# Kernel tuning notes

Measured on AMD Instinct MI355X. Metric: run time of the kernel, lower is better.

Reference implementation:

```python
import jax, jax.numpy as jnp
import numpy as np

N_NODES = 50000
N_EDGES = 800000
N_GRAPHS = 64
HEADS = 4
IN_CH, HID_CH, OUT_CH = 128, 64, 32


def setup_inputs() -> dict:
    key = jax.random.key(0)
    ks = jax.random.split(key, 13)
    x = jax.random.normal(ks[0], (N_NODES, IN_CH), dtype=jnp.float32)
    edge_index = jax.random.randint(ks[1], (2, N_EDGES), 0, N_NODES, dtype=jnp.int64)
    tensor_batch = jnp.sort(jax.random.randint(ks[2], (N_NODES,), 0, N_GRAPHS, dtype=jnp.int64))
    s = 0.1
    return {
        "x": x,
        "edge_index": edge_index,
        "tensor_batch": tensor_batch,
        "W1": jax.random.normal(ks[3], (IN_CH, HEADS * HID_CH), dtype=jnp.float32) * s,
        "a_src1": jax.random.normal(ks[4], (HEADS, HID_CH), dtype=jnp.float32) * s,
        "a_dst1": jax.random.normal(ks[5], (HEADS, HID_CH), dtype=jnp.float32) * s,
        "b1": jnp.zeros((HEADS * HID_CH,), dtype=jnp.float32),
        "W2": jax.random.normal(ks[6], (HEADS * HID_CH, HEADS * OUT_CH), dtype=jnp.float32) * s,
        "a_src2": jax.random.normal(ks[7], (HEADS, OUT_CH), dtype=jnp.float32) * s,
        "a_dst2": jax.random.normal(ks[8], (HEADS, OUT_CH), dtype=jnp.float32) * s,
        "b2": jnp.zeros((HEADS * OUT_CH,), dtype=jnp.float32),
        "Wout": jax.random.normal(ks[9], (HEADS * OUT_CH, 2), dtype=jnp.float32) * s,
        "bout": jnp.zeros((2,), dtype=jnp.float32),
    }


def gat_conv(x, src, dst, W, a_src, a_dst, b, heads, ch):
    """PyG-style GATConv (eval mode, self-loops already appended)."""
    N = x.shape[0]
    h = (x @ W).reshape(N, heads, ch)            # [N,H,C] per-head projection
    s = jnp.sum(h * a_src, axis=-1)              # [N,H] source attention term
    d = jnp.sum(h * a_dst, axis=-1)              # [N,H] dest attention term
    e = jax.nn.leaky_relu(s[src] + d[dst], negative_slope=0.2)   # [E,H]
    # segment softmax over incoming edges of each destination node
    m = jax.ops.segment_max(e, dst, num_segments=N)              # [N,H]
    ex = jnp.exp(e - m[dst])
    denom = jax.ops.segment_sum(ex, dst, num_segments=N)         # [N,H]
    alpha = ex / (denom[dst] + 1e-16)                            # [E,H]
    out = jax.ops.segment_sum(h[src] * alpha[:, :, None], dst, num_segments=N)
    return out.reshape(N, heads * ch) + b


def reference(x, edge_index, tensor_batch, W1, a_src1, a_dst1, b1,
              W2, a_src2, a_dst2, b2, Wout, bout):
    N = x.shape[0]
    loop = jnp.arange(N, dtype=edge_index.dtype)
    src = jnp.concatenate([edge_index[0], loop])  # add self-loops (PyG default)
    dst = jnp.concatenate([edge_index[1], loop])
    h = jax.nn.relu(gat_conv(x, src, dst, W1, a_src1, a_dst1, b1, HEADS, HID_CH))
    h = jax.nn.relu(gat_conv(h, src, dst, W2, a_src2, a_dst2, b2, HEADS, OUT_CH))
    # global mean pool per graph
    sums = jax.ops.segment_sum(h, tensor_batch, num_segments=N_GRAPHS)
    counts = jax.ops.segment_sum(jnp.ones((N, 1), h.dtype), tensor_batch, num_segments=N_GRAPHS)
    pooled = sums / jnp.maximum(counts, 1.0)
    logits = pooled @ Wout + bout
    return jax.nn.softmax(logits, axis=-1)
```

## Files before the change

kernel.cpp:

```cpp
#include <hip/hip_runtime.h>
#include <hip/hip_bf16.h>

#define N_NODES 50000
#define N_EDGES 800000
#define N_GRAPHS 64
#define HEADS 4
#define IN_CH 128
#define HID 64
#define F1 256
#define OUT_CH 32
#define F2 128
#define POOL_SPLITS 16
#define SCAN_B 256
#define SCAN_NB ((N_NODES + SCAN_B - 1) / SCAN_B)
#define GEMM_GRID (N_NODES / 16)
#define COUNT_GRID ((N_EDGES + 255) / 256)
#define XPACK_GRID (N_NODES * IN_CH / 8 / 256)

typedef unsigned short ushortT;
typedef unsigned int uintT;
typedef short v8s __attribute__((ext_vector_type(8)));
typedef float v4f __attribute__((ext_vector_type(4)));
typedef float v2f __attribute__((ext_vector_type(2)));

__device__ __forceinline__ ushortT f2bf(float f) {
    union { float f; unsigned int i; } v; v.f = f;
    unsigned int x = v.i;
    unsigned int r = (x + 0x7fffu + ((x >> 16) & 1u)) >> 16;
    return (ushortT)r;
}
__device__ __forceinline__ float bf_lo(uintT w) {
    union { unsigned int i; float f; } v; v.i = w << 16; return v.f;
}
__device__ __forceinline__ float bf_hi(uintT w) {
    union { unsigned int i; float f; } v; v.i = w & 0xffff0000u; return v.f;
}
__device__ __forceinline__ unsigned char f2fp8(float f) {
    return (unsigned char)__builtin_amdgcn_cvt_pk_fp8_f32(f, f, 0u, false);
}

__device__ __forceinline__ void packW_one(const float* __restrict__ W,
                                          uint4* __restrict__ dst,
                                          int i, int FIN, int FOUT) {
    int KC = FIN / 32;
    int lane = i & 63, g = i >> 6;
    int kc = g % KC, nt = g / KC;
    int n = nt * 16 + (lane & 15);
    int kbase = kc * 32 + (lane >> 4) * 8;
    union { uint4 q; ushortT u[8]; } pk;
#pragma unroll
    for (int j = 0; j < 8; j++) pk.u[j] = f2bf(W[(kbase + j) * FOUT + n]);
    dst[i] = pk.q;
}

__global__ __launch_bounds__(256) void k_pack(
        const float* __restrict__ x, const float* __restrict__ W1,
        const float* __restrict__ W2, uint4* __restrict__ wpk,
        ushortT* __restrict__ xb) {
    int b = blockIdx.x;
    if (b < 32) {
        int i = b * 256 + threadIdx.x;
        if (i < 4096) packW_one(W1, wpk, i, IN_CH, F1);
        else          packW_one(W2, wpk + 4096, i - 4096, F1, F2);
    } else {
        long i = (long)(b - 32) * 256 + threadIdx.x;
        const float4* xf = (const float4*)x + i * 2;
        float4 a = xf[0], c = xf[1];
        union { uint4 q; ushortT u[8]; } pk;
        pk.u[0] = f2bf(a.x); pk.u[1] = f2bf(a.y);
        pk.u[2] = f2bf(a.z); pk.u[3] = f2bf(a.w);
        pk.u[4] = f2bf(c.x); pk.u[5] = f2bf(c.y);
        pk.u[6] = f2bf(c.z); pk.u[7] = f2bf(c.w);
        ((uint4*)xb)[i] = pk.q;
    }
}

template <int FIN, int FOUT>
__device__ __forceinline__ void gemm_body(const ushortT* __restrict__ A,
                                          const uint4* __restrict__ Wpk,
                                          const float* __restrict__ ASrc,
                                          const float* __restrict__ ADst,
                                          unsigned char* __restrict__ out,
                                          float* __restrict__ s_out_g,
                                          float* __restrict__ d_out_g,
                                          int bid) {
    constexpr int KC = FIN / 32;
    constexpr int NTH = (FOUT / HEADS) / 16;
    int tid = threadIdx.x;
    int wave = tid >> 6, lane = tid & 63;
    long row0 = (long)bid * 16;
    int m = lane & 15, b = lane >> 4;

    v8s af[KC];
#pragma unroll
    for (int kc = 0; kc < KC; kc++) {
        union { v8s v; uint4 q; } u;
        u.q = *(const uint4*)(A + (row0 + m) * FIN + kc * 32 + b * 8);
        af[kc] = u.v;
    }

    float sp[4] = {0,0,0,0}, dp[4] = {0,0,0,0};
#pragma unroll
    for (int j = 0; j < NTH; j++) {
        int nt = wave * NTH + j;
        v4f c = {0.f, 0.f, 0.f, 0.f};
#pragma unroll
        for (int kc = 0; kc < KC; kc++) {
            union { v8s v; uint4 q; } bu;
            bu.q = Wpk[(nt * KC + kc) * 64 + lane];
            c = __builtin_amdgcn_mfma_f32_16x16x32_bf16(af[kc], bu.v, c, 0, 0, 0);
        }
        int col = nt * 16 + m;
        float av = ASrc[col], dv = ADst[col];
#pragma unroll
        for (int reg = 0; reg < 4; reg++) {
            out[(row0 + b * 4 + reg) * FOUT + col] = f2fp8(c[reg]);
            sp[reg] += c[reg] * av;
            dp[reg] += c[reg] * dv;
        }
    }
#pragma unroll
    for (int o = 1; o < 16; o <<= 1) {
#pragma unroll
        for (int reg = 0; reg < 4; reg++) {
            sp[reg] += __shfl_xor(sp[reg], o, 64);
            dp[reg] += __shfl_xor(dp[reg], o, 64);
        }
    }
    if (m == 0) {
#pragma unroll
        for (int reg = 0; reg < 4; reg++) {
            s_out_g[(row0 + b * 4 + reg) * HEADS + wave] = sp[reg];
            d_out_g[(row0 + b * 4 + reg) * HEADS + wave] = dp[reg];
        }
    }
}

__global__ __launch_bounds__(256) void k_mega1(
        const ushortT* __restrict__ xb, const uint4* __restrict__ wpk,
        const float* __restrict__ asrc1, const float* __restrict__ adst1,
        unsigned char* __restrict__ u_h, float* __restrict__ f_s,
        float* __restrict__ f_d, const int* __restrict__ ei,
        int* __restrict__ counts, int* __restrict__ rank) {
    if (blockIdx.x < GEMM_GRID) {
        gemm_body<IN_CH, F1>(xb, wpk, asrc1, adst1, u_h, f_s, f_d, blockIdx.x);
    } else {
        int e = (blockIdx.x - GEMM_GRID) * 256 + threadIdx.x;
        if (e < N_EDGES) {
            int dst = ei[N_EDGES + e];
            rank[e] = atomicAdd(&counts[dst], 1);
        }
    }
}

__global__ __launch_bounds__(256) void k_gemm2(
        const ushortT* __restrict__ A, const uint4* __restrict__ wpk2,
        const float* __restrict__ asrc2, const float* __restrict__ adst2,
        unsigned char* __restrict__ u_h, float* __restrict__ f_s,
        float* __restrict__ f_d) {
    gemm_body<F1, F2>(A, wpk2, asrc2, adst2, u_h, f_s, f_d, blockIdx.x);
}

__global__ void k_scan1(const int* __restrict__ counts, int* __restrict__ offs,
                        int* __restrict__ bsum) {
    __shared__ int sh[SCAN_B];
    int b = blockIdx.x, t = threadIdx.x;
    int i = b * SCAN_B + t;
    int v = (i < N_NODES) ? counts[i] : 0;
    sh[t] = v;
    __syncthreads();
    for (int o = 1; o < SCAN_B; o <<= 1) {
        int add = (t >= o) ? sh[t - o] : 0;
        __syncthreads();
        sh[t] += add;
        __syncthreads();
    }
    if (i < N_NODES) offs[i] = sh[t] - v;
    if (t == SCAN_B - 1) bsum[b] = sh[t];
}

__global__ void k_scan2(const int* __restrict__ bsum, int* __restrict__ bbase,
                        int* __restrict__ offs, const int* __restrict__ batch,
                        int* __restrict__ bounds) {
    __shared__ int sh[SCAN_B];
    int t = threadIdx.x;
    int v = (t < SCAN_NB) ? bsum[t] : 0;
    sh[t] = v;
    __syncthreads();
    for (int o = 1; o < SCAN_B; o <<= 1) {
        int add = (t >= o) ? sh[t - o] : 0;
        __syncthreads();
        sh[t] += add;
        __syncthreads();
    }
    if (t < SCAN_NB) bbase[t] = sh[t] - v;
    if (t == SCAN_B - 1) offs[N_NODES] = sh[t];
    if (t <= N_GRAPHS) {
        int lo = 0, hi = N_NODES;
        while (lo < hi) {
            int mid = (lo + hi) >> 1;
            if (batch[mid] < t) lo = mid + 1; else hi = mid;
        }
        bounds[t] = lo;
    }
}

__global__ void k_scatter(const int* __restrict__ ei, const int* __restrict__ offs,
                          const int* __restrict__ bbase, const int* __restrict__ rank,
                          int* __restrict__ csr_src) {
    int e = blockIdx.x * blockDim.x + threadIdx.x;
    if (e >= N_EDGES) return;
    int src = ei[e], dst = ei[N_EDGES + e];
    int pos = offs[dst] + bbase[dst >> 8] + rank[e];
    csr_src[pos] = src;
}

template <int C, int VEC, int WPB, int CHUNK>
__global__ __launch_bounds__(64 * WPB) void k_agg(
        const unsigned char* __restrict__ hb, const float* __restrict__ s,
        const float* __restrict__ d, const int* __restrict__ offs,
        const int* __restrict__ bbase, const int* __restrict__ csr_src,
        const float* __restrict__ bias, ushortT* __restrict__ xout) {
    constexpr int F = HEADS * C;
    constexpr int TPN = F / VEC;
    static_assert(TPN == 32, "two nodes per wave");
    static_assert(C / VEC == 8, "head = tl>>3");
    static_assert(N_NODES % (WPB * 2) == 0, "exact grid");
    __shared__ int lsrc[WPB][2][CHUNK];
    __shared__ float lex[WPB][2][CHUNK * HEADS];
    int wv = threadIdx.x >> 6;
    int t = threadIdx.x & 63;
    int half = t >> 5, tl = t & 31;
    int n = (blockIdx.x * WPB + wv) * 2 + half;
    int h = tl >> 3;
    int beg = offs[n] + bbase[n >> 8];
    int np1 = n + 1;
    int end = (np1 < N_NODES) ? offs[np1] + bbase[np1 >> 8] : offs[N_NODES];
    float4 dn = *(const float4*)(d + n * 4);

    float4 svn = *(const float4*)(s + n * 4);
    float ssel = (h == 0) ? svn.x : (h == 1) ? svn.y : (h == 2) ? svn.z : svn.w;
    float dsel = (h == 0) ? dn.x : (h == 1) ? dn.y : (h == 2) ? dn.z : dn.w;
    float es = ssel + dsel; es = es > 0.f ? es : 0.2f * es;
    float exs = __expf(es);
    float sumex = exs;
    float acc[VEC];
    if (VEC == 8) {
        uint2 w = ((const uint2*)hb)[(long)n * TPN + tl];
        v2f p0 = __builtin_amdgcn_cvt_pk_f32_fp8(w.x, false);
        v2f p1 = __builtin_amdgcn_cvt_pk_f32_fp8(w.x, true);
        v2f p2 = __builtin_amdgcn_cvt_pk_f32_fp8(w.y, false);
        v2f p3 = __builtin_amdgcn_cvt_pk_f32_fp8(w.y, true);
        acc[0] = exs * p0.x; acc[1] = exs * p0.y;
        acc[2] = exs * p1.x; acc[3] = exs * p1.y;
        acc[4] = exs * p2.x; acc[5] = exs * p2.y;
        acc[6] = exs * p3.x; acc[7] = exs * p3.y;
    } else {
        uintT w = ((const uintT*)hb)[(long)n * TPN + tl];
        v2f p0 = __builtin_amdgcn_cvt_pk_f32_fp8(w, false);
        v2f p1 = __builtin_amdgcn_cvt_pk_f32_fp8(w, true);
        acc[0] = exs * p0.x; acc[1] = exs * p0.y;
        acc[2] = exs * p1.x; acc[3] = exs * p1.y;
    }

    int tot = end - beg;
    int totO = __shfl_xor(tot, 32, 64);
    int maxTot = max(tot, totO);
    for (int base = 0; base < maxTot; base += CHUNK) {
        int cnt = min(CHUNK, tot - base); if (cnt < 0) cnt = 0;
        int cntW = min(CHUNK, maxTot - base);
        for (int i = tl; i < cnt; i += TPN) {
            int sn = csr_src[beg + base + i];
            lsrc[wv][half][i] = sn;
            float4 sv = *(const float4*)(s + sn * 4);
            float e0 = sv.x + dn.x; e0 = e0 > 0.f ? e0 : 0.2f * e0;
            float e1 = sv.y + dn.y; e1 = e1 > 0.f ? e1 : 0.2f * e1;
            float e2 = sv.z + dn.z; e2 = e2 > 0.f ? e2 : 0.2f * e2;
            float e3 = sv.w + dn.w; e3 = e3 > 0.f ? e3 : 0.2f * e3;
            float4 exv = { __expf(e0), __expf(e1), __expf(e2), __expf(e3) };
            *(float4*)&lex[wv][half][i * 4] = exv;
        }
        asm volatile("s_waitcnt lgkmcnt(0)" ::: "memory");
#pragma unroll 4
        for (int i = 0; i < cntW; i++) {
            bool act = i < cnt;
            float ex = act ? lex[wv][half][i * 4 + h] : 0.f;
            int sn = act ? lsrc[wv][half][i] : 0;
            sumex += ex;
            if (VEC == 8) {
                uint2 w = ((const uint2*)hb)[(long)sn * TPN + tl];
                v2f p0 = __builtin_amdgcn_cvt_pk_f32_fp8(w.x, false);
                v2f p1 = __builtin_amdgcn_cvt_pk_f32_fp8(w.x, true);
                v2f p2 = __builtin_amdgcn_cvt_pk_f32_fp8(w.y, false);
                v2f p3 = __builtin_amdgcn_cvt_pk_f32_fp8(w.y, true);
                acc[0] += ex * p0.x; acc[1] += ex * p0.y;
                acc[2] += ex * p1.x; acc[3] += ex * p1.y;
                acc[4] += ex * p2.x; acc[5] += ex * p2.y;
                acc[6] += ex * p3.x; acc[7] += ex * p3.y;
            } else {
                uintT w = ((const uintT*)hb)[(long)sn * TPN + tl];
                v2f p0 = __builtin_amdgcn_cvt_pk_f32_fp8(w, false);
                v2f p1 = __builtin_amdgcn_cvt_pk_f32_fp8(w, true);
                acc[0] += ex * p0.x; acc[1] += ex * p0.y;
                acc[2] += ex * p1.x; acc[3] += ex * p1.y;
            }
        }
        asm volatile("" ::: "memory");
    }
    float inv = 1.f / (sumex + 1e-16f);
    float o[VEC];
#pragma unroll
    for (int j = 0; j < VEC; j++)
        o[j] = fmaxf(acc[j] * inv + bias[tl * VEC + j], 0.f);
    if (VEC == 8) {
        uint4 pk;
        pk.x = (uintT)f2bf(o[0]) | ((uintT)f2bf(o[1]) << 16);
        pk.y = (uintT)f2bf(o[2]) | ((uintT)f2bf(o[3]) << 16);
        pk.z = (uintT)f2bf(o[4]) | ((uintT)f2bf(o[5]) << 16);
        pk.w = (uintT)f2bf(o[6]) | ((uintT)f2bf(o[7]) << 16);
        ((uint4*)xout)[(long)n * TPN + tl] = pk;
    } else {
        uint2 pk;
        pk.x = (uintT)f2bf(o[0]) | ((uintT)f2bf(o[1]) << 16);
        pk.y = (uintT)f2bf(o[2]) | ((uintT)f2bf(o[3]) << 16);
        ((uint2*)xout)[(long)n * TPN + tl] = pk;
    }
}

__global__ void k_pool_partial(const ushortT* __restrict__ x2, const int* __restrict__ bounds,
                               float* __restrict__ partial) {
    int g = blockIdx.x, s = blockIdx.y;
    int t = threadIdx.x;
    int n0 = bounds[g], n1 = bounds[g + 1];
    int len = n1 - n0;
    int a = n0 + (int)((long)len * s / POOL_SPLITS);
    int b = n0 + (int)((long)len * (s + 1) / POOL_SPLITS);
    float acc = 0.f;
    for (int n = a; n < b; n++) acc += bf_lo((uintT)x2[(long)n * F2 + t]);
    partial[((long)g * POOL_SPLITS + s) * F2 + t] = acc;
}

__global__ void k_head(const float* __restrict__ partial, const int* __restrict__ bounds,
                       const float* __restrict__ Wout, const float* __restrict__ bout,
                       float* __restrict__ out) {
    __shared__ float red0[F2], red1[F2];
    int g = blockIdx.x;
    int t = threadIdx.x;
    int cntN = bounds[g + 1] - bounds[g];
    float cnt = fmaxf((float)cntN, 1.0f);
    float sum = 0.f;
    for (int s = 0; s < POOL_SPLITS; s++)
        sum += partial[((long)g * POOL_SPLITS + s) * F2 + t];
    float p = sum / cnt;
    red0[t] = p * Wout[t * 2 + 0];
    red1[t] = p * Wout[t * 2 + 1];
    __syncthreads();
    for (int off = F2 / 2; off > 0; off >>= 1) {
        if (t < off) { red0[t] += red0[t + off]; red1[t] += red1[t + off]; }
        __syncthreads();
    }
    if (t == 0) {
        float l0 = red0[0] + bout[0];
        float l1 = red1[0] + bout[1];
        float m = fmaxf(l0, l1);
        float e0 = __expf(l0 - m), e1 = __expf(l1 - m);
        float inv = 1.f / (e0 + e1);
        out[g * 2 + 0] = e0 * inv;
        out[g * 2 + 1] = e1 * inv;
    }
}

extern "C" void kernel_launch(void* const* d_in, const int* in_sizes, int n_in,
                              void* d_out, int out_size, void* d_ws, size_t ws_size,
                              hipStream_t stream) {
    const float* x     = (const float*)d_in[0];
    const int*   ei    = (const int*)d_in[1];
    const int*   batch = (const int*)d_in[2];
    const float* W1    = (const float*)d_in[3];
    const float* asrc1 = (const float*)d_in[4];
    const float* adst1 = (const float*)d_in[5];
    const float* b1    = (const float*)d_in[6];
    const float* W2    = (const float*)d_in[7];
    const float* asrc2 = (const float*)d_in[8];
    const float* adst2 = (const float*)d_in[9];
    const float* b2    = (const float*)d_in[10];
    const float* Wout  = (const float*)d_in[11];
    const float* bout  = (const float*)d_in[12];

    char* ws = (char*)d_ws;
    size_t off = 0;
    auto alloc = [&](size_t bytes) -> void* {
        void* p = ws + off;
        off += (bytes + 255) / 256 * 256;
        return p;
    };
    unsigned char* u_h = (unsigned char*)alloc((size_t)N_NODES * F1);
    ushortT* u_x1  = (ushortT*)alloc(sizeof(ushortT) * (size_t)N_NODES * F1);
    ushortT* u_x2  = (ushortT*)alloc(sizeof(ushortT) * (size_t)N_NODES * F2);
    ushortT* xb    = (ushortT*)alloc(sizeof(ushortT) * (size_t)N_NODES * IN_CH);
    uint4*   wpk   = (uint4*)alloc(sizeof(uint4) * 8192);
    float*   f_s   = (float*)alloc(sizeof(float) * (size_t)N_NODES * HEADS);
    float*   f_d   = (float*)alloc(sizeof(float) * (size_t)N_NODES * HEADS);
    int*     i_cnt = (int*)alloc(sizeof(int) * (size_t)N_NODES);
    int*     i_off = (int*)alloc(sizeof(int) * (size_t)(N_NODES + 1));
    int*     i_rnk = (int*)alloc(sizeof(int) * (size_t)N_EDGES);
    int*     i_csr = (int*)alloc(sizeof(int) * (size_t)N_EDGES);
    int*     i_bnd = (int*)alloc(sizeof(int) * (size_t)(N_GRAPHS + 1));
    int*     i_bs  = (int*)alloc(sizeof(int) * SCAN_NB);
    int*     i_bb  = (int*)alloc(sizeof(int) * SCAN_NB);
    float*   f_prt = (float*)alloc(sizeof(float) * (size_t)N_GRAPHS * POOL_SPLITS * F2);
    (void)ws_size; (void)in_sizes; (void)n_in; (void)out_size;

    hipMemsetAsync(i_cnt, 0, sizeof(int) * N_NODES, stream);

    k_pack<<<32 + XPACK_GRID, 256, 0, stream>>>(x, W1, W2, wpk, xb);

    k_mega1<<<GEMM_GRID + COUNT_GRID, 256, 0, stream>>>(
        xb, wpk, asrc1, adst1, u_h, f_s, f_d, ei, i_cnt, i_rnk);

    k_scan1<<<SCAN_NB, SCAN_B, 0, stream>>>(i_cnt, i_off, i_bs);
    k_scan2<<<1, SCAN_B, 0, stream>>>(i_bs, i_bb, i_off, batch, i_bnd);
    k_scatter<<<COUNT_GRID, 256, 0, stream>>>(ei, i_off, i_bb, i_rnk, i_csr);

    int agg_grid = N_NODES / (4 * 2);

    k_agg<HID, 8, 4, 128><<<agg_grid, 256, 0, stream>>>(
        u_h, f_s, f_d, i_off, i_bb, i_csr, b1, u_x1);

    k_gemm2<<<GEMM_GRID, 256, 0, stream>>>(u_x1, wpk + 4096, asrc2, adst2,
                                           u_h, f_s, f_d);
    k_agg<OUT_CH, 4, 4, 128><<<agg_grid, 256, 0, stream>>>(
        u_h, f_s, f_d, i_off, i_bb, i_csr, b2, u_x2);

    dim3 pgrid(N_GRAPHS, POOL_SPLITS);
    k_pool_partial<<<pgrid, F2, 0, stream>>>(u_x2, i_bnd, f_prt);
    k_head<<<N_GRAPHS, F2, 0, stream>>>(f_prt, i_bnd, Wout, bout, (float*)d_out);
}
```

Before: 277.4 us.

## Partition edge-count atomics into 16 per-slice histograms and schedule counting first

Edge degree counting now uses 16 separate count arrays, one per contiguous slice of edges, so atomics on the same destination are spread across more addresses. The scan kernel first turns these per-slice counts into per-slice prefix offsets, and the scatter kernel adds the slice offset. The counting blocks are also moved ahead of the GEMM blocks in the fused launch so they start earlier. The cost is a 16x larger count buffer with a bigger memset and 16 strided reads and writes per node in the scan.

```diff
diff --git a/kernel.cpp b/kernel.cpp
--- a/kernel.cpp
+++ b/kernel.cpp
@@ -16,6 +16,8 @@
 #define GEMM_GRID (N_NODES / 16)
 #define COUNT_GRID ((N_EDGES + 255) / 256)
 #define XPACK_GRID (N_NODES * IN_CH / 8 / 256)
+#define NP 16
+#define EPP (N_EDGES / NP)
 
 typedef unsigned short ushortT;
 typedef unsigned int uintT;
@@ -141,15 +143,17 @@
         const float* __restrict__ asrc1, const float* __restrict__ adst1,
         unsigned char* __restrict__ u_h, float* __restrict__ f_s,
         float* __restrict__ f_d, const int* __restrict__ ei,
-        int* __restrict__ counts, int* __restrict__ rank) {
-    if (blockIdx.x < GEMM_GRID) {
-        gemm_body<IN_CH, F1>(xb, wpk, asrc1, adst1, u_h, f_s, f_d, blockIdx.x);
-    } else {
-        int e = (blockIdx.x - GEMM_GRID) * 256 + threadIdx.x;
+        int* __restrict__ cp, int* __restrict__ rank) {
+    if (blockIdx.x < COUNT_GRID) {
+        int e = blockIdx.x * 256 + threadIdx.x;
         if (e < N_EDGES) {
             int dst = ei[N_EDGES + e];
-            rank[e] = atomicAdd(&counts[dst], 1);
-        }
+            int p = e / EPP;
+            rank[e] = atomicAdd(&cp[p * N_NODES + dst], 1);
+        }
+    } else {
+        gemm_body<IN_CH, F1>(xb, wpk, asrc1, adst1, u_h, f_s, f_d,
+                             blockIdx.x - COUNT_GRID);
     }
 }
 
@@ -161,12 +165,22 @@
     gemm_body<F1, F2>(A, wpk2, asrc2, adst2, u_h, f_s, f_d, blockIdx.x);
 }
 
-__global__ void k_scan1(const int* __restrict__ counts, int* __restrict__ offs,
+__global__ void k_scan1(int* __restrict__ cp, int* __restrict__ offs,
                         int* __restrict__ bsum) {
     __shared__ int sh[SCAN_B];
     int b = blockIdx.x, t = threadIdx.x;
     int i = b * SCAN_B + t;
-    int v = (i < N_NODES) ? counts[i] : 0;
+    int v = 0;
+    if (i < N_NODES) {
+        int run = 0;
+#pragma unroll
+        for (int p = 0; p < NP; p++) {
+            int c = cp[p * N_NODES + i];
+            cp[p * N_NODES + i] = run;
+            run += c;
+        }
+        v = run;
+    }
     sh[t] = v;
     __syncthreads();
     for (int o = 1; o < SCAN_B; o <<= 1) {
@@ -207,11 +221,12 @@
 
 __global__ void k_scatter(const int* __restrict__ ei, const int* __restrict__ offs,
                           const int* __restrict__ bbase, const int* __restrict__ rank,
-                          int* __restrict__ csr_src) {
+                          const int* __restrict__ cp, int* __restrict__ csr_src) {
     int e = blockIdx.x * blockDim.x + threadIdx.x;
     if (e >= N_EDGES) return;
     int src = ei[e], dst = ei[N_EDGES + e];
-    int pos = offs[dst] + bbase[dst >> 8] + rank[e];
+    int p = e / EPP;
+    int pos = offs[dst] + bbase[dst >> 8] + cp[p * N_NODES + dst] + rank[e];
     csr_src[pos] = src;
 }
 
@@ -401,7 +416,7 @@
     uint4*   wpk   = (uint4*)alloc(sizeof(uint4) * 8192);
     float*   f_s   = (float*)alloc(sizeof(float) * (size_t)N_NODES * HEADS);
     float*   f_d   = (float*)alloc(sizeof(float) * (size_t)N_NODES * HEADS);
-    int*     i_cnt = (int*)alloc(sizeof(int) * (size_t)N_NODES);
+    int*     i_cp  = (int*)alloc(sizeof(int) * (size_t)NP * N_NODES);
     int*     i_off = (int*)alloc(sizeof(int) * (size_t)(N_NODES + 1));
     int*     i_rnk = (int*)alloc(sizeof(int) * (size_t)N_EDGES);
     int*     i_csr = (int*)alloc(sizeof(int) * (size_t)N_EDGES);
@@ -411,16 +426,16 @@
     float*   f_prt = (float*)alloc(sizeof(float) * (size_t)N_GRAPHS * POOL_SPLITS * F2);
     (void)ws_size; (void)in_sizes; (void)n_in; (void)out_size;
 
-    hipMemsetAsync(i_cnt, 0, sizeof(int) * N_NODES, stream);
+    hipMemsetAsync(i_cp, 0, sizeof(int) * (size_t)NP * N_NODES, stream);
 
     k_pack<<<32 + XPACK_GRID, 256, 0, stream>>>(x, W1, W2, wpk, xb);
 
-    k_mega1<<<GEMM_GRID + COUNT_GRID, 256, 0, stream>>>(
-        xb, wpk, asrc1, adst1, u_h, f_s, f_d, ei, i_cnt, i_rnk);
-
-    k_scan1<<<SCAN_NB, SCAN_B, 0, stream>>>(i_cnt, i_off, i_bs);
+    k_mega1<<<COUNT_GRID + GEMM_GRID, 256, 0, stream>>>(
+        xb, wpk, asrc1, adst1, u_h, f_s, f_d, ei, i_cp, i_rnk);
+
+    k_scan1<<<SCAN_NB, SCAN_B, 0, stream>>>(i_cp, i_off, i_bs);
     k_scan2<<<1, SCAN_B, 0, stream>>>(i_bs, i_bb, i_off, batch, i_bnd);
-    k_scatter<<<COUNT_GRID, 256, 0, stream>>>(ei, i_off, i_bb, i_rnk, i_csr);
+    k_scatter<<<COUNT_GRID, 256, 0, stream>>>(ei, i_off, i_bb, i_rnk, i_cp, i_csr);
 
     int agg_grid = N_NODES / (4 * 2);
 
```

New measurement: 279.9 us. About the same (+0.9%).

## Fuse x bf16 conversion into GEMM, give each wave full rows, fold memset

Applied to the files above, without the earlier changes.

The fp32 input is now converted to bf16 inside the first GEMM instead of a separate pack pass, which removes a kernel and a bf16 staging buffer. The GEMM mapping changes so each wave owns 16 rows and computes all output column tiles across every head, rather than four waves sharing 16 rows, and the attention partials are reduced per head inside the loop. The counts memset moves into the weight-pack kernel. In exchange, each wave now streams the whole packed weight matrix and issues more MFMAs serially, and the fp32 loads in the GEMM are scalar and uncoalesced.

```diff
diff --git a/kernel.cpp b/kernel.cpp
--- a/kernel.cpp
+++ b/kernel.cpp
@@ -13,9 +13,8 @@
 #define POOL_SPLITS 16
 #define SCAN_B 256
 #define SCAN_NB ((N_NODES + SCAN_B - 1) / SCAN_B)
-#define GEMM_GRID (N_NODES / 16)
+#define GEMM_GRID ((N_NODES + 63) / 64)
 #define COUNT_GRID ((N_EDGES + 255) / 256)
-#define XPACK_GRID (N_NODES * IN_CH / 8 / 256)
 
 typedef unsigned short ushortT;
 typedef unsigned int uintT;
@@ -53,56 +52,58 @@
     dst[i] = pk.q;
 }
 
-__global__ __launch_bounds__(256) void k_pack(
-        const float* __restrict__ x, const float* __restrict__ W1,
-        const float* __restrict__ W2, uint4* __restrict__ wpk,
-        ushortT* __restrict__ xb) {
-    int b = blockIdx.x;
-    if (b < 32) {
-        int i = b * 256 + threadIdx.x;
-        if (i < 4096) packW_one(W1, wpk, i, IN_CH, F1);
-        else          packW_one(W2, wpk + 4096, i - 4096, F1, F2);
-    } else {
-        long i = (long)(b - 32) * 256 + threadIdx.x;
-        const float4* xf = (const float4*)x + i * 2;
-        float4 a = xf[0], c = xf[1];
-        union { uint4 q; ushortT u[8]; } pk;
-        pk.u[0] = f2bf(a.x); pk.u[1] = f2bf(a.y);
-        pk.u[2] = f2bf(a.z); pk.u[3] = f2bf(a.w);
-        pk.u[4] = f2bf(c.x); pk.u[5] = f2bf(c.y);
-        pk.u[6] = f2bf(c.z); pk.u[7] = f2bf(c.w);
-        ((uint4*)xb)[i] = pk.q;
-    }
-}
-
-template <int FIN, int FOUT>
-__device__ __forceinline__ void gemm_body(const ushortT* __restrict__ A,
+__global__ __launch_bounds__(256) void k_packw(
+        const float* __restrict__ W1, const float* __restrict__ W2,
+        uint4* __restrict__ wpk, int* __restrict__ counts) {
+    int i = blockIdx.x * 256 + threadIdx.x;
+    if (i < 4096) packW_one(W1, wpk, i, IN_CH, F1);
+    else          packW_one(W2, wpk + 4096, i - 4096, F1, F2);
+    for (int j = i; j < N_NODES; j += 8192) counts[j] = 0;
+}
+
+template <int FIN, int FOUT, bool ABF16>
+__device__ __forceinline__ void gemm_body(const void* __restrict__ A,
                                           const uint4* __restrict__ Wpk,
                                           const float* __restrict__ ASrc,
                                           const float* __restrict__ ADst,
                                           unsigned char* __restrict__ out,
                                           float* __restrict__ s_out_g,
                                           float* __restrict__ d_out_g,
-                                          int bid) {
+                                          int nrows, int bid) {
     constexpr int KC = FIN / 32;
+    constexpr int NT = FOUT / 16;
     constexpr int NTH = (FOUT / HEADS) / 16;
     int tid = threadIdx.x;
     int wave = tid >> 6, lane = tid & 63;
-    long row0 = (long)bid * 16;
+    long row0 = (long)bid * 64 + wave * 16;
+    if (row0 >= nrows) return;
     int m = lane & 15, b = lane >> 4;
 
     v8s af[KC];
-#pragma unroll
-    for (int kc = 0; kc < KC; kc++) {
-        union { v8s v; uint4 q; } u;
-        u.q = *(const uint4*)(A + (row0 + m) * FIN + kc * 32 + b * 8);
-        af[kc] = u.v;
+    if (ABF16) {
+        const ushortT* Ab = (const ushortT*)A;
+#pragma unroll
+        for (int kc = 0; kc < KC; kc++) {
+            union { v8s v; uint4 q; } u;
+            u.q = *(const uint4*)(Ab + (row0 + m) * FIN + kc * 32 + b * 8);
+            af[kc] = u.v;
+        }
+    } else {
+        const float* Af = (const float*)A;
+#pragma unroll
+        for (int kc = 0; kc < KC; kc++) {
+            union { v8s v; ushortT u[8]; } u;
+            const float* p = Af + (row0 + m) * FIN + kc * 32 + b * 8;
+#pragma unroll
+            for (int j = 0; j < 8; j++) u.u[j] = f2bf(p[j]);
+            af[kc] = u.v;
+        }
     }
 
     float sp[4] = {0,0,0,0}, dp[4] = {0,0,0,0};
-#pragma unroll
-    for (int j = 0; j < NTH; j++) {
-        int nt = wave * NTH + j;
+    float sk[4], dk[4];
+#pragma unroll
+    for (int nt = 0; nt < NT; nt++) {
         v4f c = {0.f, 0.f, 0.f, 0.f};
 #pragma unroll
         for (int kc = 0; kc < KC; kc++) {
@@ -112,38 +113,49 @@
         }
         int col = nt * 16 + m;
         float av = ASrc[col], dv = ADst[col];
+        long r0 = row0 + b * 4;
 #pragma unroll
         for (int reg = 0; reg < 4; reg++) {
-            out[(row0 + b * 4 + reg) * FOUT + col] = f2fp8(c[reg]);
+            out[(r0 + reg) * FOUT + col] = f2fp8(c[reg]);
             sp[reg] += c[reg] * av;
             dp[reg] += c[reg] * dv;
         }
-    }
-#pragma unroll
-    for (int o = 1; o < 16; o <<= 1) {
+        if ((nt % NTH) == NTH - 1) {
+#pragma unroll
+            for (int o = 1; o < 16; o <<= 1) {
+#pragma unroll
+                for (int reg = 0; reg < 4; reg++) {
+                    sp[reg] += __shfl_xor(sp[reg], o, 64);
+                    dp[reg] += __shfl_xor(dp[reg], o, 64);
+                }
+            }
+            int hd = nt / NTH;
+#pragma unroll
+            for (int reg = 0; reg < 4; reg++) {
+                if (m == hd) { sk[reg] = sp[reg]; dk[reg] = dp[reg]; }
+                sp[reg] = 0.f; dp[reg] = 0.f;
+            }
+        }
+    }
+    if (m < HEADS) {
+        long r0 = row0 + b * 4;
 #pragma unroll
         for (int reg = 0; reg < 4; reg++) {
-            sp[reg] += __shfl_xor(sp[reg], o, 64);
-            dp[reg] += __shfl_xor(dp[reg], o, 64);
-        }
-    }
-    if (m == 0) {
-#pragma unroll
-        for (int reg = 0; reg < 4; reg++) {
-            s_out_g[(row0 + b * 4 + reg) * HEADS + wave] = sp[reg];
-            d_out_g[(row0 + b * 4 + reg) * HEADS + wave] = dp[reg];
+            s_out_g[(r0 + reg) * HEADS + m] = sk[reg];
+            d_out_g[(r0 + reg) * HEADS + m] = dk[reg];
         }
     }
 }
 
 __global__ __launch_bounds__(256) void k_mega1(
-        const ushortT* __restrict__ xb, const uint4* __restrict__ wpk,
+        const float* __restrict__ x, const uint4* __restrict__ wpk,
         const float* __restrict__ asrc1, const float* __restrict__ adst1,
         unsigned char* __restrict__ u_h, float* __restrict__ f_s,
         float* __restrict__ f_d, const int* __restrict__ ei,
         int* __restrict__ counts, int* __restrict__ rank) {
     if (blockIdx.x < GEMM_GRID) {
-        gemm_body<IN_CH, F1>(xb, wpk, asrc1, adst1, u_h, f_s, f_d, blockIdx.x);
+        gemm_body<IN_CH, F1, false>(x, wpk, asrc1, adst1, u_h, f_s, f_d,
+                                    N_NODES, blockIdx.x);
     } else {
         int e = (blockIdx.x - GEMM_GRID) * 256 + threadIdx.x;
         if (e < N_EDGES) {
@@ -158,7 +170,8 @@
         const float* __restrict__ asrc2, const float* __restrict__ adst2,
         unsigned char* __restrict__ u_h, float* __restrict__ f_s,
         float* __restrict__ f_d) {
-    gemm_body<F1, F2>(A, wpk2, asrc2, adst2, u_h, f_s, f_d, blockIdx.x);
+    gemm_body<F1, F2, true>(A, wpk2, asrc2, adst2, u_h, f_s, f_d,
+                            N_NODES, blockIdx.x);
 }
 
 __global__ void k_scan1(const int* __restrict__ counts, int* __restrict__ offs,
@@ -397,7 +410,6 @@
     unsigned char* u_h = (unsigned char*)alloc((size_t)N_NODES * F1);
     ushortT* u_x1  = (ushortT*)alloc(sizeof(ushortT) * (size_t)N_NODES * F1);
     ushortT* u_x2  = (ushortT*)alloc(sizeof(ushortT) * (size_t)N_NODES * F2);
-    ushortT* xb    = (ushortT*)alloc(sizeof(ushortT) * (size_t)N_NODES * IN_CH);
     uint4*   wpk   = (uint4*)alloc(sizeof(uint4) * 8192);
     float*   f_s   = (float*)alloc(sizeof(float) * (size_t)N_NODES * HEADS);
     float*   f_d   = (float*)alloc(sizeof(float) * (size_t)N_NODES * HEADS);
@@ -411,12 +423,10 @@
     float*   f_prt = (float*)alloc(sizeof(float) * (size_t)N_GRAPHS * POOL_SPLITS * F2);
     (void)ws_size; (void)in_sizes; (void)n_in; (void)out_size;
 
-    hipMemsetAsync(i_cnt, 0, sizeof(int) * N_NODES, stream);
-
-    k_pack<<<32 + XPACK_GRID, 256, 0, stream>>>(x, W1, W2, wpk, xb);
+    k_packw<<<32, 256, 0, stream>>>(W1, W2, wpk, i_cnt);
 
     k_mega1<<<GEMM_GRID + COUNT_GRID, 256, 0, stream>>>(
-        xb, wpk, asrc1, adst1, u_h, f_s, f_d, ei, i_cnt, i_rnk);
+        x, wpk, asrc1, adst1, u_h, f_s, f_d, ei, i_cnt, i_rnk);
 
     k_scan1<<<SCAN_NB, SCAN_B, 0, stream>>>(i_cnt, i_off, i_bs);
     k_scan2<<<1, SCAN_B, 0, stream>>>(i_bs, i_bb, i_off, batch, i_bnd);
```

After: 254.7 us. -8.2%, faster.
